# Kernel optimization log

Hardware: AMD Instinct MI355X
Metric: run time of the kernel (lower is better)

The kernel has to match this reference:

```python
import jax, jax.numpy as jnp
import numpy as np

SIM_THRESHOLD = 0.65  # recall() returns decoded memory only if best_sim > 0.65
EPS = 1e-8            # torch F.cosine_similarity default eps


def setup_inputs() -> dict:
    key = jax.random.key(0)
    k1, k2, k3, k4 = jax.random.split(key, 4)
    dim, seq, n_mem = 1024, 2048, 131072
    bound = 1.0 / np.sqrt(dim)  # nn.Linear default init scale
    return {
        "query": jax.random.normal(k1, (seq, dim), dtype=jnp.float32),
        "bank": jax.random.normal(k2, (n_mem, dim), dtype=jnp.float32),
        "w_dec": jax.random.uniform(k3, (dim, dim), dtype=jnp.float32, minval=-bound, maxval=bound),
        "b_dec": jax.random.uniform(k4, (dim,), dtype=jnp.float32, minval=-bound, maxval=bound),
    }


def reference(query, bank, w_dec, b_dec):
    # q = query.detach().mean(dim=0)
    q = query.mean(axis=0)                                   # [dim]
    # cosine similarity of q against every stored memory (batched version of
    # the per-item F.cosine_similarity loop): dot / (max(||a||,eps)*max(||b||,eps))
    q_norm = jnp.maximum(jnp.linalg.norm(q), EPS)
    bank_norms = jnp.maximum(jnp.linalg.norm(bank, axis=1), EPS)  # [N]
    sims = (bank @ q) / (bank_norms * q_norm)                 # [N]
    idx = jnp.argmax(sims)
    best_sim = sims[idx]
    best_mem = bank[idx]                                      # [dim]
    # decoder(best.embedding): Linear(dim, dim)
    decoded = best_mem @ w_dec.T + b_dec                      # [dim]
    # original returns None below threshold; model as zeros to keep static shape
    return jnp.where(best_sim > SIM_THRESHOLD, decoded, jnp.zeros_like(decoded))
```

## Files before the change

kernel.cpp:

```cpp
#include <hip/hip_runtime.h>

#define EPS 1e-8f
#define THR 0.65f

constexpr int DIM  = 1024;
constexpr int SEQ  = 2048;
constexpr int NMEM = 131072;

constexpr int NCOPY     = 8;
constexpr int SIM_BLKS  = 2048;

constexpr int WS_Q     = 8192;
constexpr int WS_QNORM = 9216;
constexpr int WS_BESTS = 9218;
constexpr int WS_FINAL = 13314;

__global__ void init_kernel(float* __restrict__ ws) {
    ((float4*)ws)[blockIdx.x * 256 + threadIdx.x] = make_float4(0.f, 0.f, 0.f, 0.f);
}

__global__ void qsum_kernel(const float* __restrict__ query, float* __restrict__ ws) {
    const float4* q4 = (const float4*)query;
    int tid = threadIdx.x;
    int r0  = blockIdx.x * 8;
    float4 s = make_float4(0.f, 0.f, 0.f, 0.f);
    #pragma unroll
    for (int r = 0; r < 8; ++r) {
        float4 v = q4[(size_t)(r0 + r) * 256 + tid];
        s.x += v.x; s.y += v.y; s.z += v.z; s.w += v.w;
    }
    float* dst = ws + (blockIdx.x & (NCOPY - 1)) * DIM + tid * 4;
    atomicAdd(dst + 0, s.x);
    atomicAdd(dst + 1, s.y);
    atomicAdd(dst + 2, s.z);
    atomicAdd(dst + 3, s.w);
}

__global__ void qfinal_kernel(float* __restrict__ ws) {
    __shared__ float red[4];
    int tid = threadIdx.x;
    float4 v = make_float4(0.f, 0.f, 0.f, 0.f);
    #pragma unroll
    for (int c = 0; c < NCOPY; ++c) {
        float4 p = ((float4*)ws)[c * 256 + tid];
        v.x += p.x; v.y += p.y; v.z += p.z; v.w += p.w;
    }
    const float inv = 1.0f / (float)SEQ;
    v.x *= inv; v.y *= inv; v.z *= inv; v.w *= inv;
    ((float4*)(ws + WS_Q))[tid] = v;
    float ss = v.x * v.x + v.y * v.y + v.z * v.z + v.w * v.w;
    #pragma unroll
    for (int m = 32; m >= 1; m >>= 1) ss += __shfl_xor(ss, m);
    int lane = tid & 63, wid = tid >> 6;
    if (lane == 0) red[wid] = ss;
    __syncthreads();
    if (tid == 0) {
        float tot = red[0] + red[1] + red[2] + red[3];
        ws[WS_QNORM] = fmaxf(sqrtf(tot), EPS);
    }
}

__device__ __forceinline__ unsigned int float_to_ordered(float f) {
    unsigned int b = __float_as_uint(f);
    return (b & 0x80000000u) ? ~b : (b | 0x80000000u);
}

__device__ __forceinline__ unsigned long long pack_best(float sim, int idx) {
    return ((unsigned long long)float_to_ordered(sim) << 32) |
           (unsigned int)(~(unsigned int)idx);
}

__launch_bounds__(256)
__global__ void sim_kernel(const float* __restrict__ bank, const float* __restrict__ ws,
                           unsigned long long* __restrict__ bests) {
    __shared__ unsigned long long wbest[4];
    int tid  = threadIdx.x;
    int lane = tid & 63;
    int wid  = tid >> 6;

    const float4* q4 = (const float4*)(ws + WS_Q);
    float4 q0 = q4[lane +   0];
    float4 q1 = q4[lane +  64];
    float4 q2 = q4[lane + 128];
    float4 q3 = q4[lane + 192];
    float qn = ws[WS_QNORM];

    int gw = blockIdx.x * 4 + wid;
    int nw = gridDim.x * 4;

    float bestSim = -1e30f;
    int   bestIdx = 0;

    for (int row = gw; row < NMEM; row += nw) {
        const float4* bp = (const float4*)(bank + (size_t)row * DIM);
        float4 b0 = bp[lane +   0];
        float4 b1 = bp[lane +  64];
        float4 b2 = bp[lane + 128];
        float4 b3 = bp[lane + 192];
        float dot = b0.x*q0.x + b0.y*q0.y + b0.z*q0.z + b0.w*q0.w
                  + b1.x*q1.x + b1.y*q1.y + b1.z*q1.z + b1.w*q1.w
                  + b2.x*q2.x + b2.y*q2.y + b2.z*q2.z + b2.w*q2.w
                  + b3.x*q3.x + b3.y*q3.y + b3.z*q3.z + b3.w*q3.w;
        float ss  = b0.x*b0.x + b0.y*b0.y + b0.z*b0.z + b0.w*b0.w
                  + b1.x*b1.x + b1.y*b1.y + b1.z*b1.z + b1.w*b1.w
                  + b2.x*b2.x + b2.y*b2.y + b2.z*b2.z + b2.w*b2.w
                  + b3.x*b3.x + b3.y*b3.y + b3.z*b3.z + b3.w*b3.w;
        #pragma unroll
        for (int m = 32; m >= 1; m >>= 1) {
            dot += __shfl_xor(dot, m);
            ss  += __shfl_xor(ss, m);
        }
        float bn  = fmaxf(sqrtf(ss), EPS);
        float sim = dot / (bn * qn);
        if (sim > bestSim) { bestSim = sim; bestIdx = row; }
    }
    if (lane == 0) wbest[wid] = pack_best(bestSim, bestIdx);
    __syncthreads();
    if (tid == 0) {
        unsigned long long p = wbest[0];
        if (wbest[1] > p) p = wbest[1];
        if (wbest[2] > p) p = wbest[2];
        if (wbest[3] > p) p = wbest[3];
        bests[blockIdx.x] = p;
    }
}

__global__ void bestfinal_kernel(const unsigned long long* __restrict__ bests,
                                 unsigned long long* __restrict__ final_best) {
    __shared__ unsigned long long red[256];
    int tid = threadIdx.x;
    unsigned long long p = bests[tid];
    #pragma unroll
    for (int i = 1; i < SIM_BLKS / 256; ++i) {
        unsigned long long v = bests[tid + i * 256];
        if (v > p) p = v;
    }
    red[tid] = p;
    __syncthreads();
    #pragma unroll
    for (int s = 128; s >= 1; s >>= 1) {
        if (tid < s) {
            if (red[tid + s] > red[tid]) red[tid] = red[tid + s];
        }
        __syncthreads();
    }
    if (tid == 0) *final_best = red[0];
}

__global__ void decode_kernel(const float* __restrict__ bank,
                              const float* __restrict__ w_dec,
                              const float* __restrict__ b_dec,
                              const unsigned long long* __restrict__ best,
                              float* __restrict__ out) {
    __shared__ float mem[DIM];
    int tid = threadIdx.x;

    unsigned long long p = *best;
    unsigned int u = (unsigned int)(p >> 32);
    unsigned int fb = (u & 0x80000000u) ? (u & 0x7FFFFFFFu) : ~u;
    float sim = __uint_as_float(fb);
    int idx   = (int)(~(unsigned int)(p & 0xFFFFFFFFu));

    ((float4*)mem)[tid] = ((const float4*)(bank + (size_t)idx * DIM))[tid];
    __syncthreads();

    bool ok  = sim > THR;
    int lane = tid & 63, wid = tid >> 6;
    int row  = blockIdx.x * 4 + wid;

    const float4* wp = (const float4*)(w_dec + (size_t)row * DIM);
    const float4* m4 = (const float4*)mem;
    float dot = 0.f;
    #pragma unroll
    for (int it = 0; it < 4; ++it) {
        float4 w = wp[lane + it * 64];
        float4 m = m4[lane + it * 64];
        dot += w.x * m.x + w.y * m.y + w.z * m.z + w.w * m.w;
    }
    #pragma unroll
    for (int m = 32; m >= 1; m >>= 1) dot += __shfl_xor(dot, m);

    if (lane == 0) out[row] = ok ? (dot + b_dec[row]) : 0.0f;
}

extern "C" void kernel_launch(void* const* d_in, const int* in_sizes, int n_in,
                              void* d_out, int out_size, void* d_ws, size_t ws_size,
                              hipStream_t stream) {
    const float* query = (const float*)d_in[0];
    const float* bank  = (const float*)d_in[1];
    const float* w_dec = (const float*)d_in[2];
    const float* b_dec = (const float*)d_in[3];
    float* out = (float*)d_out;
    float* ws  = (float*)d_ws;
    unsigned long long* bests      = (unsigned long long*)(ws + WS_BESTS);
    unsigned long long* final_best = (unsigned long long*)(ws + WS_FINAL);

    init_kernel<<<NCOPY, 256, 0, stream>>>(ws);
    qsum_kernel<<<SEQ / 8, 256, 0, stream>>>(query, ws);
    qfinal_kernel<<<1, 256, 0, stream>>>(ws);
    sim_kernel<<<SIM_BLKS, 256, 0, stream>>>(bank, ws, bests);
    bestfinal_kernel<<<1, 256, 0, stream>>>(bests, final_best);
    decode_kernel<<<256, 256, 0, stream>>>(bank, w_dec, b_dec, final_best, out);
}
```

Measured before the change: 111.8 us.

## Batch contiguous row loads with nontemporal hints and fuse final argmax into decode

Each wave now processes a contiguous chunk of bank rows, loading four rows at once with nontemporal loads to raise memory-level parallelism on the bandwidth-bound similarity scan. The separate final-argmax kernel is removed and every decode block redundantly reduces the per-block bests itself, saving a launch. This adds register pressure and redundant reduction work across 256 decode blocks.

Result: no change. 110.6 us (-1.1%).

```diff
diff --git a/kernel.cpp b/kernel.cpp
--- a/kernel.cpp
+++ b/kernel.cpp
@@ -7,13 +7,15 @@
 constexpr int SEQ  = 2048;
 constexpr int NMEM = 131072;
 
-constexpr int NCOPY     = 8;
-constexpr int SIM_BLKS  = 2048;
+constexpr int NCOPY    = 8;
+constexpr int SIM_BLKS = 2048;
+constexpr int ROWS_PER_WAVE = NMEM / (SIM_BLKS * 4);
+
+typedef float f4 __attribute__((ext_vector_type(4)));
 
 constexpr int WS_Q     = 8192;
 constexpr int WS_QNORM = 9216;
 constexpr int WS_BESTS = 9218;
-constexpr int WS_FINAL = 13314;
 
 __global__ void init_kernel(float* __restrict__ ws) {
     ((float4*)ws)[blockIdx.x * 256 + threadIdx.x] = make_float4(0.f, 0.f, 0.f, 0.f);
@@ -70,7 +72,7 @@
            (unsigned int)(~(unsigned int)idx);
 }
 
-__launch_bounds__(256)
+__launch_bounds__(256, 4)
 __global__ void sim_kernel(const float* __restrict__ bank, const float* __restrict__ ws,
                            unsigned long long* __restrict__ bests) {
     __shared__ unsigned long long wbest[4];
@@ -78,42 +80,58 @@
     int lane = tid & 63;
     int wid  = tid >> 6;
 
-    const float4* q4 = (const float4*)(ws + WS_Q);
-    float4 q0 = q4[lane +   0];
-    float4 q1 = q4[lane +  64];
-    float4 q2 = q4[lane + 128];
-    float4 q3 = q4[lane + 192];
+    const f4* q4 = (const f4*)(ws + WS_Q);
+    f4 q0 = q4[lane +   0];
+    f4 q1 = q4[lane +  64];
+    f4 q2 = q4[lane + 128];
+    f4 q3 = q4[lane + 192];
     float qn = ws[WS_QNORM];
 
-    int gw = blockIdx.x * 4 + wid;
-    int nw = gridDim.x * 4;
+    int gw   = blockIdx.x * 4 + wid;
+    int row0 = gw * ROWS_PER_WAVE;
 
     float bestSim = -1e30f;
     int   bestIdx = 0;
 
-    for (int row = gw; row < NMEM; row += nw) {
-        const float4* bp = (const float4*)(bank + (size_t)row * DIM);
-        float4 b0 = bp[lane +   0];
-        float4 b1 = bp[lane +  64];
-        float4 b2 = bp[lane + 128];
-        float4 b3 = bp[lane + 192];
-        float dot = b0.x*q0.x + b0.y*q0.y + b0.z*q0.z + b0.w*q0.w
-                  + b1.x*q1.x + b1.y*q1.y + b1.z*q1.z + b1.w*q1.w
-                  + b2.x*q2.x + b2.y*q2.y + b2.z*q2.z + b2.w*q2.w
-                  + b3.x*q3.x + b3.y*q3.y + b3.z*q3.z + b3.w*q3.w;
-        float ss  = b0.x*b0.x + b0.y*b0.y + b0.z*b0.z + b0.w*b0.w
-                  + b1.x*b1.x + b1.y*b1.y + b1.z*b1.z + b1.w*b1.w
-                  + b2.x*b2.x + b2.y*b2.y + b2.z*b2.z + b2.w*b2.w
-                  + b3.x*b3.x + b3.y*b3.y + b3.z*b3.z + b3.w*b3.w;
+    #pragma unroll
+    for (int g = 0; g < ROWS_PER_WAVE / 4; ++g) {
+        float dot[4], ss[4];
+        f4 b[4][4];
+        #pragma unroll
+        for (int r = 0; r < 4; ++r) {
+            const f4* bp = (const f4*)(bank + (size_t)(row0 + g * 4 + r) * DIM);
+            b[r][0] = __builtin_nontemporal_load(bp + lane +   0);
+            b[r][1] = __builtin_nontemporal_load(bp + lane +  64);
+            b[r][2] = __builtin_nontemporal_load(bp + lane + 128);
+            b[r][3] = __builtin_nontemporal_load(bp + lane + 192);
+        }
+        #pragma unroll
+        for (int r = 0; r < 4; ++r) {
+            dot[r] = b[r][0].x*q0.x + b[r][0].y*q0.y + b[r][0].z*q0.z + b[r][0].w*q0.w
+                   + b[r][1].x*q1.x + b[r][1].y*q1.y + b[r][1].z*q1.z + b[r][1].w*q1.w
+                   + b[r][2].x*q2.x + b[r][2].y*q2.y + b[r][2].z*q2.z + b[r][2].w*q2.w
+                   + b[r][3].x*q3.x + b[r][3].y*q3.y + b[r][3].z*q3.z + b[r][3].w*q3.w;
+            ss[r]  = b[r][0].x*b[r][0].x + b[r][0].y*b[r][0].y + b[r][0].z*b[r][0].z + b[r][0].w*b[r][0].w
+                   + b[r][1].x*b[r][1].x + b[r][1].y*b[r][1].y + b[r][1].z*b[r][1].z + b[r][1].w*b[r][1].w
+                   + b[r][2].x*b[r][2].x + b[r][2].y*b[r][2].y + b[r][2].z*b[r][2].z + b[r][2].w*b[r][2].w
+                   + b[r][3].x*b[r][3].x + b[r][3].y*b[r][3].y + b[r][3].z*b[r][3].z + b[r][3].w*b[r][3].w;
+        }
         #pragma unroll
         for (int m = 32; m >= 1; m >>= 1) {
-            dot += __shfl_xor(dot, m);
-            ss  += __shfl_xor(ss, m);
-        }
-        float bn  = fmaxf(sqrtf(ss), EPS);
-        float sim = dot / (bn * qn);
-        if (sim > bestSim) { bestSim = sim; bestIdx = row; }
-    }
+            #pragma unroll
+            for (int r = 0; r < 4; ++r) {
+                dot[r] += __shfl_xor(dot[r], m);
+                ss[r]  += __shfl_xor(ss[r], m);
+            }
+        }
+        #pragma unroll
+        for (int r = 0; r < 4; ++r) {
+            float bn  = fmaxf(sqrtf(ss[r]), EPS);
+            float sim = dot[r] / (bn * qn);
+            if (sim > bestSim) { bestSim = sim; bestIdx = row0 + g * 4 + r; }
+        }
+    }
+
     if (lane == 0) wbest[wid] = pack_best(bestSim, bestIdx);
     __syncthreads();
     if (tid == 0) {
@@ -125,10 +143,15 @@
     }
 }
 
-__global__ void bestfinal_kernel(const unsigned long long* __restrict__ bests,
-                                 unsigned long long* __restrict__ final_best) {
+__global__ void decode_kernel(const float* __restrict__ bank,
+                              const float* __restrict__ w_dec,
+                              const float* __restrict__ b_dec,
+                              const unsigned long long* __restrict__ bests,
+                              float* __restrict__ out) {
     __shared__ unsigned long long red[256];
+    __shared__ float mem[DIM];
     int tid = threadIdx.x;
+
     unsigned long long p = bests[tid];
     #pragma unroll
     for (int i = 1; i < SIM_BLKS / 256; ++i) {
@@ -144,18 +167,7 @@
         }
         __syncthreads();
     }
-    if (tid == 0) *final_best = red[0];
-}
-
-__global__ void decode_kernel(const float* __restrict__ bank,
-                              const float* __restrict__ w_dec,
-                              const float* __restrict__ b_dec,
-                              const unsigned long long* __restrict__ best,
-                              float* __restrict__ out) {
-    __shared__ float mem[DIM];
-    int tid = threadIdx.x;
-
-    unsigned long long p = *best;
+    p = red[0];
     unsigned int u = (unsigned int)(p >> 32);
     unsigned int fb = (u & 0x80000000u) ? (u & 0x7FFFFFFFu) : ~u;
     float sim = __uint_as_float(fb);
@@ -192,13 +204,11 @@
     const float* b_dec = (const float*)d_in[3];
     float* out = (float*)d_out;
     float* ws  = (float*)d_ws;
-    unsigned long long* bests      = (unsigned long long*)(ws + WS_BESTS);
-    unsigned long long* final_best = (unsigned long long*)(ws + WS_FINAL);
+    unsigned long long* bests = (unsigned long long*)(ws + WS_BESTS);
 
     init_kernel<<<NCOPY, 256, 0, stream>>>(ws);
     qsum_kernel<<<SEQ / 8, 256, 0, stream>>>(query, ws);
     qfinal_kernel<<<1, 256, 0, stream>>>(ws);
     sim_kernel<<<SIM_BLKS, 256, 0, stream>>>(bank, ws, bests);
-    bestfinal_kernel<<<1, 256, 0, stream>>>(bests, final_best);
-    decode_kernel<<<256, 256, 0, stream>>>(bank, w_dec, b_dec, final_best, out);
-}
+    decode_kernel<<<256, 256, 0, stream>>>(bank, w_dec, b_dec, bests, out);
+}
```
